# Performance work log

Measured on AMD Instinct MI355X. Metric: run time of the kernel, lower is better.

## Reference

```python
import jax, jax.numpy as jnp
import numpy as np

TEMPERATURE = 0.1


def setup_inputs() -> dict:
    key = jax.random.key(0)
    k1, k2 = jax.random.split(key)
    B, D = 4096, 256
    z_i = jax.random.normal(k1, (B, D), dtype=jnp.float32)
    z_j = jax.random.normal(k2, (B, D), dtype=jnp.float32)
    return {"z_i": z_i, "z_j": z_j}


def reference(z_i, z_j):
    B = z_i.shape[0]
    N = 2 * B
    z = jnp.concatenate([z_i, z_j], axis=0)  # [N, D]
    # cosine similarity via normalize + GEMM (same math as broadcasted F.cosine_similarity)
    eps = 1e-8
    zn = z / jnp.maximum(jnp.linalg.norm(z, axis=1, keepdims=True), eps)
    sim = (zn @ zn.T) / TEMPERATURE  # [N, N]
    # positives: sim[i, (i+B) % N]
    rows = jnp.arange(N)
    pos = sim[rows, (rows + B) % N]  # [N]
    # denominator: sum of exp over all entries except the diagonal (positives included,
    # matching the original which only masks the eye)
    neg_inf = jnp.array(-jnp.inf, sim.dtype)
    sim_masked = jnp.where(jnp.eye(N, dtype=bool), neg_inf, sim)
    lse = jax.nn.logsumexp(sim_masked, axis=1)  # [N]
    loss = -(pos - lse)
    return loss.mean()
```

## Files before the change

kernel.cpp:

```cpp
#include <hip/hip_runtime.h>
#include <hip/hip_bf16.h>

typedef __bf16 bf16x8 __attribute__((ext_vector_type(8)));
typedef float  f32x16 __attribute__((ext_vector_type(16)));

#define N_TOT  8192
#define B_HALF 4096
#define D      256
#define SQK1   3.79828254f
#define LN2    0.6931471805599453f

#define RB      256
#define WROWS   64
#define CB      32
#define SLICE   512
#define NSLICE  16
#define NSTAGE  16
#define LDS_RS  264

__global__ __launch_bounds__(256) void normalize_kernel(
    const float* __restrict__ zi, const float* __restrict__ zj,
    ushort* __restrict__ zn, float* __restrict__ out)
{
    if (blockIdx.x == 0 && threadIdx.x == 0) *out = 0.0f;
    int row  = (blockIdx.x * 256 + threadIdx.x) >> 6;
    int lane = threadIdx.x & 63;
    const float* src = (row < B_HALF) ? (zi + (size_t)row * D)
                                      : (zj + (size_t)(row - B_HALF) * D);
    float4 v = ((const float4*)src)[lane];
    float ss = v.x * v.x + v.y * v.y + v.z * v.z + v.w * v.w;
    #pragma unroll
    for (int m = 1; m < 64; m <<= 1) ss += __shfl_xor(ss, m);
    float r = SQK1 / fmaxf(sqrtf(ss), 1e-8f);
    union { ushort4 u4; __hip_bfloat16 h[4]; } o;
    o.h[0] = __float2bfloat16(v.x * r);
    o.h[1] = __float2bfloat16(v.y * r);
    o.h[2] = __float2bfloat16(v.z * r);
    o.h[3] = __float2bfloat16(v.w * r);
    ((ushort4*)zn)[(size_t)row * (D / 4) + lane] = o.u4;
}

__global__ __launch_bounds__(256) void fused_kernel(
    const ushort* __restrict__ zn,
    float* __restrict__ spartial,
    float* __restrict__ posdot)
{
    __shared__ ushort lds[2][CB * LDS_RS];

    int tid  = threadIdx.x;
    int lane = tid & 63;
    int w    = tid >> 6;
    int hi   = lane >> 5;
    int c32  = lane & 31;
    int r0   = blockIdx.x * RB + w * WROWS;
    int cs0  = blockIdx.y * SLICE;

    bf16x8 a[2][16];
    #pragma unroll
    for (int rt = 0; rt < 2; ++rt) {
        const ushort* ar = zn + (size_t)(r0 + rt * 32 + c32) * D + hi * 8;
        #pragma unroll
        for (int ks = 0; ks < 16; ++ks)
            a[rt][ks] = *(const bf16x8*)(ar + ks * 16);
    }

    float srow[2][16];
    #pragma unroll
    for (int rt = 0; rt < 2; ++rt)
        #pragma unroll
        for (int g = 0; g < 16; ++g) srow[rt][g] = 0.f;

    uint4 st[4];
    #pragma unroll
    for (int i = 0; i < 4; ++i) {
        int chunk = tid + i * 256;
        st[i] = *(const uint4*)(zn + (size_t)(cs0 + (chunk >> 5)) * D + (chunk & 31) * 8);
    }
    #pragma unroll
    for (int i = 0; i < 4; ++i) {
        int chunk = tid + i * 256;
        *(uint4*)(&lds[0][(chunk >> 5) * LDS_RS + (chunk & 31) * 8]) = st[i];
    }
    __syncthreads();

    for (int s = 0; s < NSTAGE; ++s) {
        int cur = s & 1;
        if (s + 1 < NSTAGE) {
            #pragma unroll
            for (int i = 0; i < 4; ++i) {
                int chunk = tid + i * 256;
                st[i] = *(const uint4*)(zn + (size_t)(cs0 + (s + 1) * CB + (chunk >> 5)) * D + (chunk & 31) * 8);
            }
        }

        f32x16 acc0 = {};
        f32x16 acc1 = {};
        const ushort* bbase = &lds[cur][(size_t)c32 * LDS_RS + hi * 8];
        __builtin_amdgcn_s_setprio(1);
        #pragma unroll
        for (int ks = 0; ks < 16; ++ks) {
            bf16x8 b = *(const bf16x8*)(bbase + ks * 16);
            asm volatile("v_mfma_f32_32x32x16_bf16 %0, %1, %2, %0"
                         : "+v"(acc0) : "a"(a[0][ks]), "v"(b));
            asm volatile("v_mfma_f32_32x32x16_bf16 %0, %1, %2, %0"
                         : "+v"(acc1) : "a"(a[1][ks]), "v"(b));
        }
        __builtin_amdgcn_s_setprio(0);

        int colbase = cs0 + s * CB;
        #pragma unroll
        for (int rt = 0; rt < 2; ++rt) {
            const f32x16& acc = (rt == 0) ? acc0 : acc1;
            int rowbase = r0 + rt * 32;
            bool isdiag = (rowbase == colbase);
            bool ispos  = ((rowbase ^ B_HALF) == colbase);
            if (isdiag) {
                #pragma unroll
                for (int g = 0; g < 16; ++g) {
                    int rl = (g & 3) + 8 * (g >> 2) + 4 * hi;
                    float e = exp2f(acc[g]);
                    srow[rt][g] += (rl != c32) ? e : 0.0f;
                }
            } else if (ispos) {
                #pragma unroll
                for (int g = 0; g < 16; ++g) {
                    int rl = (g & 3) + 8 * (g >> 2) + 4 * hi;
                    if (rl == c32) posdot[rowbase + rl] = acc[g];
                    srow[rt][g] += exp2f(acc[g]);
                }
            } else {
                #pragma unroll
                for (int g = 0; g < 16; ++g)
                    srow[rt][g] += exp2f(acc[g]);
            }
        }

        if (s + 1 < NSTAGE) {
            __syncthreads();
            #pragma unroll
            for (int i = 0; i < 4; ++i) {
                int chunk = tid + i * 256;
                *(uint4*)(&lds[cur ^ 1][(chunk >> 5) * LDS_RS + (chunk & 31) * 8]) = st[i];
            }
            __syncthreads();
        }
    }

    #pragma unroll
    for (int rt = 0; rt < 2; ++rt) {
        #pragma unroll
        for (int g = 0; g < 16; ++g) {
            float v = srow[rt][g];
            v += __shfl_xor(v, 1);
            v += __shfl_xor(v, 2);
            v += __shfl_xor(v, 4);
            v += __shfl_xor(v, 8);
            v += __shfl_xor(v, 16);
            if (c32 == 0) {
                int rl = (g & 3) + 8 * (g >> 2) + 4 * hi;
                spartial[(size_t)(r0 + rt * 32 + rl) * NSLICE + blockIdx.y] = v;
            }
        }
    }
}

__global__ __launch_bounds__(256) void finalize_kernel(
    const float* __restrict__ spartial, const float* __restrict__ posdot,
    float* __restrict__ out)
{
    int i    = blockIdx.x * 256 + threadIdx.x;
    int lane = threadIdx.x & 63;
    int wv   = threadIdx.x >> 6;
    float ssum = 0.f;
    #pragma unroll
    for (int k = 0; k < NSLICE; ++k) ssum += spartial[(size_t)i * NSLICE + k];
    float loss = LN2 * (log2f(ssum) - posdot[i]);
    #pragma unroll
    for (int m = 1; m < 64; m <<= 1) loss += __shfl_xor(loss, m);
    __shared__ float red[4];
    if (lane == 0) red[wv] = loss;
    __syncthreads();
    if (threadIdx.x == 0) {
        float t = red[0] + red[1] + red[2] + red[3];
        atomicAdd(out, t * (1.0f / (float)N_TOT));
    }
}

extern "C" void kernel_launch(void* const* d_in, const int* in_sizes, int n_in,
                              void* d_out, int out_size, void* d_ws, size_t ws_size,
                              hipStream_t stream)
{
    const float* zi = (const float*)d_in[0];
    const float* zj = (const float*)d_in[1];
    float* out = (float*)d_out;

    ushort* zn       = (ushort*)d_ws;
    float*  posdot   = (float*)((char*)d_ws + (size_t)N_TOT * D * 2);
    float*  spartial = (float*)((char*)d_ws + (size_t)N_TOT * D * 2 + N_TOT * 4);

    normalize_kernel<<<N_TOT / 4, 256, 0, stream>>>(zi, zj, zn, out);

    dim3 grid2(N_TOT / RB, NSLICE);
    fused_kernel<<<grid2, 256, 0, stream>>>(zn, spartial, posdot);

    finalize_kernel<<<N_TOT / 256, 256, 0, stream>>>(spartial, posdot, out);
}
```

Before: 122.7 us.

## Switch fused kernel to 16x16x32 MFMA tiles with smaller row blocks and swizzled LDS

Replaces the 32x32x16 bf16 MFMA path with 16x16x32 MFMA intrinsics. Each wave now covers 32 rows instead of 64, and each block 128 rows instead of 256, which doubles the grid's row dimension. The padded LDS row stride becomes an XOR swizzle so that B-fragment reads avoid bank conflicts without padding. The aim is fewer registers per thread, more blocks for occupancy, and conflict-free LDS access. In exchange, each column tile staged in LDS is reused by half as many rows, so there are relatively more global loads and barriers per unit of MFMA work.

```diff
diff --git a/kernel.cpp b/kernel.cpp
--- a/kernel.cpp
+++ b/kernel.cpp
@@ -2,7 +2,7 @@
 #include <hip/hip_bf16.h>
 
 typedef __bf16 bf16x8 __attribute__((ext_vector_type(8)));
-typedef float  f32x16 __attribute__((ext_vector_type(16)));
+typedef float  f32x4  __attribute__((ext_vector_type(4)));
 
 #define N_TOT  8192
 #define B_HALF 4096
@@ -10,13 +10,12 @@
 #define SQK1   3.79828254f
 #define LN2    0.6931471805599453f
 
-#define RB      256
-#define WROWS   64
+#define RB      128
+#define WROWS   32
 #define CB      32
 #define SLICE   512
 #define NSLICE  16
 #define NSTAGE  16
-#define LDS_RS  264
 
 __global__ __launch_bounds__(256) void normalize_kernel(
     const float* __restrict__ zi, const float* __restrict__ zj,
@@ -45,30 +44,30 @@
     float* __restrict__ spartial,
     float* __restrict__ posdot)
 {
-    __shared__ ushort lds[2][CB * LDS_RS];
+    __shared__ ushort lds[2][CB * 256];
 
     int tid  = threadIdx.x;
     int lane = tid & 63;
     int w    = tid >> 6;
-    int hi   = lane >> 5;
-    int c32  = lane & 31;
+    int l15  = lane & 15;
+    int l4   = lane >> 4;
     int r0   = blockIdx.x * RB + w * WROWS;
     int cs0  = blockIdx.y * SLICE;
 
-    bf16x8 a[2][16];
+    bf16x8 a[2][8];
     #pragma unroll
     for (int rt = 0; rt < 2; ++rt) {
-        const ushort* ar = zn + (size_t)(r0 + rt * 32 + c32) * D + hi * 8;
-        #pragma unroll
-        for (int ks = 0; ks < 16; ++ks)
-            a[rt][ks] = *(const bf16x8*)(ar + ks * 16);
-    }
-
-    float srow[2][16];
+        const ushort* ar = zn + (size_t)(r0 + rt * 16 + l15) * D + l4 * 8;
+        #pragma unroll
+        for (int kc = 0; kc < 8; ++kc)
+            a[rt][kc] = *(const bf16x8*)(ar + kc * 32);
+    }
+
+    float srow[2][4];
     #pragma unroll
     for (int rt = 0; rt < 2; ++rt)
         #pragma unroll
-        for (int g = 0; g < 16; ++g) srow[rt][g] = 0.f;
+        for (int g = 0; g < 4; ++g) srow[rt][g] = 0.f;
 
     uint4 st[4];
     #pragma unroll
@@ -79,9 +78,12 @@
     #pragma unroll
     for (int i = 0; i < 4; ++i) {
         int chunk = tid + i * 256;
-        *(uint4*)(&lds[0][(chunk >> 5) * LDS_RS + (chunk & 31) * 8]) = st[i];
+        int col = chunk >> 5, k16 = chunk & 31;
+        *(uint4*)(&lds[0][col * 256 + ((k16 * 8) ^ ((col & 7) << 3))]) = st[i];
     }
     __syncthreads();
+
+    int swzr = (lane & 7) << 3;
 
     for (int s = 0; s < NSTAGE; ++s) {
         int cur = s & 1;
@@ -93,45 +95,47 @@
             }
         }
 
-        f32x16 acc0 = {};
-        f32x16 acc1 = {};
-        const ushort* bbase = &lds[cur][(size_t)c32 * LDS_RS + hi * 8];
+        f32x4 acc[2][2] = {};
         __builtin_amdgcn_s_setprio(1);
         #pragma unroll
-        for (int ks = 0; ks < 16; ++ks) {
-            bf16x8 b = *(const bf16x8*)(bbase + ks * 16);
-            asm volatile("v_mfma_f32_32x32x16_bf16 %0, %1, %2, %0"
-                         : "+v"(acc0) : "a"(a[0][ks]), "v"(b));
-            asm volatile("v_mfma_f32_32x32x16_bf16 %0, %1, %2, %0"
-                         : "+v"(acc1) : "a"(a[1][ks]), "v"(b));
+        for (int kc = 0; kc < 8; ++kc) {
+            #pragma unroll
+            for (int ct = 0; ct < 2; ++ct) {
+                int col = ct * 16 + l15;
+                bf16x8 b = *(const bf16x8*)(&lds[cur][col * 256 + ((kc * 32 + l4 * 8) ^ swzr)]);
+                acc[0][ct] = __builtin_amdgcn_mfma_f32_16x16x32_bf16(a[0][kc], b, acc[0][ct], 0, 0, 0);
+                acc[1][ct] = __builtin_amdgcn_mfma_f32_16x16x32_bf16(a[1][kc], b, acc[1][ct], 0, 0, 0);
+            }
         }
         __builtin_amdgcn_s_setprio(0);
 
-        int colbase = cs0 + s * CB;
         #pragma unroll
         for (int rt = 0; rt < 2; ++rt) {
-            const f32x16& acc = (rt == 0) ? acc0 : acc1;
-            int rowbase = r0 + rt * 32;
-            bool isdiag = (rowbase == colbase);
-            bool ispos  = ((rowbase ^ B_HALF) == colbase);
-            if (isdiag) {
-                #pragma unroll
-                for (int g = 0; g < 16; ++g) {
-                    int rl = (g & 3) + 8 * (g >> 2) + 4 * hi;
-                    float e = exp2f(acc[g]);
-                    srow[rt][g] += (rl != c32) ? e : 0.0f;
+            int rowb = r0 + rt * 16;
+            #pragma unroll
+            for (int ct = 0; ct < 2; ++ct) {
+                int colb = cs0 + s * CB + ct * 16;
+                bool isdiag = (rowb == colb);
+                bool ispos  = ((rowb ^ B_HALF) == colb);
+                if (isdiag) {
+                    #pragma unroll
+                    for (int g = 0; g < 4; ++g) {
+                        int rl = l4 * 4 + g;
+                        float e = exp2f(acc[rt][ct][g]);
+                        srow[rt][g] += (rl != l15) ? e : 0.0f;
+                    }
+                } else if (ispos) {
+                    #pragma unroll
+                    for (int g = 0; g < 4; ++g) {
+                        int rl = l4 * 4 + g;
+                        if (rl == l15) posdot[rowb + rl] = acc[rt][ct][g];
+                        srow[rt][g] += exp2f(acc[rt][ct][g]);
+                    }
+                } else {
+                    #pragma unroll
+                    for (int g = 0; g < 4; ++g)
+                        srow[rt][g] += exp2f(acc[rt][ct][g]);
                 }
-            } else if (ispos) {
-                #pragma unroll
-                for (int g = 0; g < 16; ++g) {
-                    int rl = (g & 3) + 8 * (g >> 2) + 4 * hi;
-                    if (rl == c32) posdot[rowbase + rl] = acc[g];
-                    srow[rt][g] += exp2f(acc[g]);
-                }
-            } else {
-                #pragma unroll
-                for (int g = 0; g < 16; ++g)
-                    srow[rt][g] += exp2f(acc[g]);
             }
         }
 
@@ -140,7 +144,8 @@
             #pragma unroll
             for (int i = 0; i < 4; ++i) {
                 int chunk = tid + i * 256;
-                *(uint4*)(&lds[cur ^ 1][(chunk >> 5) * LDS_RS + (chunk & 31) * 8]) = st[i];
+                int col = chunk >> 5, k16 = chunk & 31;
+                *(uint4*)(&lds[cur ^ 1][col * 256 + ((k16 * 8) ^ ((col & 7) << 3))]) = st[i];
             }
             __syncthreads();
         }
@@ -149,16 +154,15 @@
     #pragma unroll
     for (int rt = 0; rt < 2; ++rt) {
         #pragma unroll
-        for (int g = 0; g < 16; ++g) {
+        for (int g = 0; g < 4; ++g) {
             float v = srow[rt][g];
             v += __shfl_xor(v, 1);
             v += __shfl_xor(v, 2);
             v += __shfl_xor(v, 4);
             v += __shfl_xor(v, 8);
-            v += __shfl_xor(v, 16);
-            if (c32 == 0) {
-                int rl = (g & 3) + 8 * (g >> 2) + 4 * hi;
-                spartial[(size_t)(r0 + rt * 32 + rl) * NSLICE + blockIdx.y] = v;
+            if (l15 == 0) {
+                int row = r0 + rt * 16 + l4 * 4 + g;
+                spartial[(size_t)row * NSLICE + blockIdx.y] = v;
             }
         }
     }
```

New measurement: 142.9 us. 16.4% more time.
